# Optimization experiments

Hardware: AMD Instinct MI355X
Metric: run time of the kernel (lower is better)

Reference implementation:

```python
import jax, jax.numpy as jnp
import numpy as np

N = 100_000   # nodes
E = 3_200_000 # directed edges
EC = 16       # edge_channels

def setup_inputs() -> dict:
    key = jax.random.key(0)
    ks = jax.random.split(key, 9)
    x = jax.random.normal(ks[0], (N, 8), jnp.float32)
    adjs = jax.random.randint(ks[1], (2, E), 0, N, jnp.int32)
    edge_attr = jax.random.normal(ks[2], (E, EC), jnp.float32)
    s = 1.0 / np.sqrt(EC)
    lin_e_w = jax.random.uniform(ks[3], (1, EC), jnp.float32, -s, s)
    lin_e_b = jax.random.uniform(ks[4], (1,), jnp.float32, -s, s)
    aggr2_w = jax.random.uniform(ks[5], (1, 4), jnp.float32, -0.5, 0.5)
    aggr2_b = jax.random.uniform(ks[6], (1,), jnp.float32, -0.5, 0.5)
    lin_l_w = jax.random.uniform(ks[7], (1, 1), jnp.float32, -1.0, 1.0)
    lin_l_b = jax.random.uniform(ks[8], (1,), jnp.float32, -1.0, 1.0)
    return dict(x=x, adjs=adjs, edge_attr=edge_attr,
                lin_e_w=lin_e_w, lin_e_b=lin_e_b,
                aggr2_w=aggr2_w, aggr2_b=aggr2_b,
                lin_l_w=lin_l_w, lin_l_b=lin_l_b)

def reference(x, adjs, edge_attr, lin_e_w, lin_e_b, aggr2_w, aggr2_b, lin_l_w, lin_l_b):
    n = x.shape[0]
    # layer 0 (EdgeConv): edge MLP edge_channels -> 1
    ev = (edge_attr @ lin_e_w.T + lin_e_b)[:, 0]            # [E]
    src, dst = adjs[0], adjs[1]
    # to_undirected: edges + reversed edges; row 1 (scatter dest) = cat(dst, src)
    u_idx = jnp.concatenate([dst, src])                      # [2E]
    u_val = jnp.concatenate([ev, ev])                        # [2E]
    cnt = jax.ops.segment_sum(jnp.ones_like(u_val), u_idx, num_segments=n)
    nsum = jax.ops.segment_sum(u_val, u_idx, num_segments=n)
    nmax = jnp.where(cnt > 0, jax.ops.segment_max(u_val, u_idx, num_segments=n), 0.0)
    nmin = jnp.where(cnt > 0, jax.ops.segment_min(u_val, u_idx, num_segments=n), 0.0)
    nmean = nsum / jnp.maximum(cnt, 1.0)                     # torch-scatter mean: 0 for empty

    def inv_clean(node_vals):
        r = 1.0 / node_vals[dst]                             # propagate -> x_i = x[edge_index[1]]
        return jnp.where(jnp.isnan(r) | (r == jnp.inf), 1.0, r)

    nc = jnp.stack([inv_clean(nmax), inv_clean(nmean), inv_clean(nmin), inv_clean(nsum)], axis=1)  # [E,4]
    ec = jnp.where(jnp.isnan(ev) | (ev == jnp.inf), 1.0, ev)[:, None]   # cleaned edge_attr [E,1]
    nc2 = nc @ aggr2_w.T + aggr2_b                            # [E,1]
    out = (ec @ lin_l_w.T + lin_l_b) + nc2 * ec               # [E,1]
    out = jnp.where(out == jnp.inf, 1.0, out)
    return out.reshape(-1)                                    # torch.flatten
```

## Files before the change

kernel.cpp:

```cpp
#include <hip/hip_runtime.h>

#define INF_F (__builtin_inff())
#define PMAX 512
#define G1 1024
#define BT 512
#define BT4 1024
#define NPART 256
#define MARKER 0xFFFFFFFFu
#define LREC 9856


__device__ __forceinline__ unsigned int enc_f(float f) {
    unsigned int u = __float_as_uint(f);
    return (u & 0x80000000u) ? ~u : (u | 0x80000000u);
}
__device__ __forceinline__ float dec_f(unsigned int u) {
    unsigned int b = (u & 0x80000000u) ? (u & 0x7FFFFFFFu) : ~u;
    return __uint_as_float(b);
}
__device__ __forceinline__ float inv_clean(float x) {
    float r = 1.0f / x;
    if (isnan(r) || r == INF_F) r = 1.0f;
    return r;
}
__device__ __forceinline__ float edge_final(float ev, float c, float lw, float lb) {
    float ec = (isnan(ev) || ev == INF_F) ? 1.0f : ev;
    float out = ec * lw + lb + c * ec;
    if (out == INF_F) out = 1.0f;
    return out;
}
__device__ __forceinline__ float dot16_bias(const float* __restrict__ edge_attr,
                                            const float* __restrict__ lin_e_w,
                                            const float* __restrict__ lin_e_b, int e) {
    const float4* ea = reinterpret_cast<const float4*>(edge_attr) + (size_t)e * 4;
    const float4* w4 = reinterpret_cast<const float4*>(lin_e_w);
    float4 a0 = ea[0], a1 = ea[1], a2 = ea[2], a3 = ea[3];
    float4 w0 = w4[0], w1 = w4[1], w2 = w4[2], w3 = w4[3];
    return a0.x * w0.x + a0.y * w0.y + a0.z * w0.z + a0.w * w0.w
         + a1.x * w1.x + a1.y * w1.y + a1.z * w1.z + a1.w * w1.w
         + a2.x * w2.x + a2.y * w2.y + a2.z * w2.z + a2.w * w2.w
         + a3.x * w3.x + a3.y * w3.y + a3.z * w3.z + a3.w * w3.w
         + lin_e_b[0];
}


__global__ void __launch_bounds__(BT)
k1_ev_count(const float* __restrict__ edge_attr,
            const int* __restrict__ src, const int* __restrict__ dst,
            const float* __restrict__ lin_e_w, const float* __restrict__ lin_e_b,
            float* __restrict__ ev_out, unsigned int* __restrict__ gh,
            int E, int P, int CE) {
    __shared__ unsigned int hist[PMAX];
    int t = threadIdx.x, b = blockIdx.x;
    for (int p = t; p < P; p += BT) hist[p] = 0u;
    __syncthreads();
    int start = b * CE, end = min(E, start + CE);
    for (int e = start + t; e < end; e += BT) {
        float ev = dot16_bias(edge_attr, lin_e_w, lin_e_b, e);
        ev_out[e] = ev;
        atomicAdd(&hist[(unsigned int)src[e] >> 8], 1u);
        atomicAdd(&hist[(unsigned int)dst[e] >> 8], 1u);
    }
    __syncthreads();
    for (int p = t; p < P; p += BT) gh[(size_t)b * P + p] = hist[p];
}

__global__ void __launch_bounds__(256)
k2_scan_cols(unsigned int* __restrict__ gh, unsigned int* __restrict__ ptotal, int P) {
    const int VPT = G1 / 256;
    int p = blockIdx.x, t = threadIdx.x;
    unsigned int v[VPT], s = 0u;
    #pragma unroll
    for (int i = 0; i < VPT; ++i) {
        v[i] = (gh[(size_t)(t * VPT + i) * P + p] + 7u) & ~7u;
        s += v[i];
    }
    __shared__ unsigned int sc[256];
    sc[t] = s;
    __syncthreads();
    for (int off = 1; off < 256; off <<= 1) {
        unsigned int x = (t >= off) ? sc[t - off] : 0u;
        __syncthreads();
        sc[t] += x;
        __syncthreads();
    }
    unsigned int run = sc[t] - s;
    #pragma unroll
    for (int i = 0; i < VPT; ++i) {
        gh[(size_t)(t * VPT + i) * P + p] = run;
        run += v[i];
    }
    if (t == 255) ptotal[p] = run;
}

__global__ void k3_scan_part(const unsigned int* __restrict__ ptotal,
                             unsigned int* __restrict__ pbase, int P) {
    int t = threadIdx.x;
    unsigned int u0 = (2 * t < P) ? ptotal[2 * t] : 0u;
    unsigned int u1 = (2 * t + 1 < P) ? ptotal[2 * t + 1] : 0u;
    unsigned int s = u0 + u1;
    __shared__ unsigned int sc[256];
    sc[t] = s;
    __syncthreads();
    for (int off = 1; off < 256; off <<= 1) {
        unsigned int x = (t >= off) ? sc[t - off] : 0u;
        __syncthreads();
        sc[t] += x;
        __syncthreads();
    }
    unsigned int excl = sc[t] - s;
    if (2 * t < P) pbase[2 * t] = excl;
    if (2 * t + 1 < P) pbase[2 * t + 1] = excl + u0;
}

__global__ void __launch_bounds__(BT4)
k4_staged(const int* __restrict__ src, const int* __restrict__ dst,
          const float* __restrict__ ev_in,
          const unsigned int* __restrict__ gh, const unsigned int* __restrict__ pbase,
          const unsigned int* __restrict__ ptotal,
          uint2* __restrict__ rec, int E, int P, int CE) {
    __shared__ uint2 lrec[LREC];
    __shared__ unsigned int lstart[PMAX + 1];
    __shared__ unsigned int lcur[PMAX];
    __shared__ unsigned int goff[PMAX];
    __shared__ unsigned int sc[512];

    const int t = threadIdx.x, b = blockIdx.x;

    for (int p = t; p < P; p += BT4) {
        unsigned int g0 = gh[(size_t)b * P + p];
        unsigned int g1 = (b + 1 < G1) ? gh[(size_t)(b + 1) * P + p] : ptotal[p];
        lcur[p] = g1 - g0;
        goff[p] = pbase[p] + g0;
    }
    __syncthreads();

    unsigned int v = (t < P) ? lcur[t] : 0u;
    if (t < 512) sc[t] = v;
    __syncthreads();
    for (int off = 1; off < 512; off <<= 1) {
        unsigned int x = 0u;
        if (t < 512 && t >= off) x = sc[t - off];
        __syncthreads();
        if (t < 512) sc[t] += x;
        __syncthreads();
    }
    if (t < P) { lstart[t] = sc[t] - v; lcur[t] = sc[t] - v; }
    if (t == P - 1) lstart[P] = sc[t];
    __syncthreads();

    const int start = b * CE, end = min(E, start + CE);
    for (int e = start + t; e < end; e += BT4) {
        float ev = ev_in[e];
        unsigned int ebits = __float_as_uint(ev);
        unsigned int s = (unsigned int)src[e], d = (unsigned int)dst[e];
        unsigned int pos = atomicAdd(&lcur[d >> 8], 1u);
        lrec[pos] = make_uint2(ebits, d & 255u);
        pos = atomicAdd(&lcur[s >> 8], 1u);
        lrec[pos] = make_uint2(ebits, s & 255u);
    }
    __syncthreads();

    for (int p = t; p < P; p += BT4)
        for (unsigned int q = lcur[p]; q < lstart[p + 1]; ++q)
            lrec[q] = make_uint2(0u, MARKER);
    __syncthreads();

    const unsigned int tot = lstart[P];
    for (unsigned int j = t; j < tot; j += BT4) {
        int lo = 0, hi = P;
        while (hi - lo > 1) {
            int mid = (lo + hi) >> 1;
            if (lstart[mid] <= j) lo = mid; else hi = mid;
        }
        rec[goff[lo] + (j - lstart[lo])] = lrec[j];
    }
}

__global__ void __launch_bounds__(1024)
k5_reduce(const uint2* __restrict__ rec,
          const unsigned int* __restrict__ pbase, const unsigned int* __restrict__ ptotal,
          const float* __restrict__ aggr2_w, const float* __restrict__ aggr2_b,
          float* __restrict__ nodeC, int N) {
    __shared__ float ssum[NPART];
    __shared__ unsigned int scnt[NPART], smax[NPART], smin[NPART];
    int p = blockIdx.x, t = threadIdx.x;
    if (t < NPART) { ssum[t] = 0.0f; scnt[t] = 0u; smax[t] = 0u; smin[t] = 0xFFFFFFFFu; }
    __syncthreads();
    unsigned int pb = pbase[p], tot = ptotal[p];
    const uint4* r4 = reinterpret_cast<const uint4*>(rec + pb);
    unsigned int n4 = tot >> 1;
    for (unsigned int i = t; i < n4; i += 1024) {
        uint4 q = r4[i];
        if (q.y != MARKER) {
            float v = __uint_as_float(q.x);
            unsigned int eu = enc_f(v);
            atomicAdd(&ssum[q.y], v);
            atomicAdd(&scnt[q.y], 1u);
            atomicMax(&smax[q.y], eu);
            atomicMin(&smin[q.y], eu);
        }
        if (q.w != MARKER) {
            float v = __uint_as_float(q.z);
            unsigned int eu = enc_f(v);
            atomicAdd(&ssum[q.w], v);
            atomicAdd(&scnt[q.w], 1u);
            atomicMax(&smax[q.w], eu);
            atomicMin(&smin[q.w], eu);
        }
    }
    __syncthreads();
    int node = p * NPART + t;
    if (t < NPART && node < N) {
        unsigned int c = scnt[t];
        float sum = ssum[t];
        float mxv = (c > 0u) ? dec_f(smax[t]) : 0.0f;
        float mnv = (c > 0u) ? dec_f(smin[t]) : 0.0f;
        float mean = sum / fmaxf((float)c, 1.0f);
        float4 w = *reinterpret_cast<const float4*>(aggr2_w);
        nodeC[node] = w.x * inv_clean(mxv) + w.y * inv_clean(mean)
                    + w.z * inv_clean(mnv) + w.w * inv_clean(sum) + aggr2_b[0];
    }
}

__global__ void __launch_bounds__(256)
edge_out(float* __restrict__ evout, const int* __restrict__ dst,
         const float* __restrict__ nodeC,
         const float* __restrict__ lin_l_w, const float* __restrict__ lin_l_b,
         int E) {
    int i = blockIdx.x * blockDim.x + threadIdx.x;
    int base = i * 4;
    float lw = lin_l_w[0], lb = lin_l_b[0];
    if (base + 3 < E) {
        float4 ev = *reinterpret_cast<const float4*>(evout + base);
        int4 d = *reinterpret_cast<const int4*>(dst + base);
        float4 o;
        o.x = edge_final(ev.x, nodeC[d.x], lw, lb);
        o.y = edge_final(ev.y, nodeC[d.y], lw, lb);
        o.z = edge_final(ev.z, nodeC[d.z], lw, lb);
        o.w = edge_final(ev.w, nodeC[d.w], lw, lb);
        *reinterpret_cast<float4*>(evout + base) = o;
    } else {
        for (int e = base; e < E; ++e)
            evout[e] = edge_final(evout[e], nodeC[dst[e]], lw, lb);
    }
}


__global__ void init_nodes_fb(unsigned long long* __restrict__ sc,
                              unsigned int* __restrict__ mx,
                              unsigned int* __restrict__ mn, int total) {
    int i = blockIdx.x * blockDim.x + threadIdx.x;
    if (i < total) { sc[i] = 0ull; mx[i] = 0u; mn[i] = 0xFFFFFFFFu; }
}

__global__ void __launch_bounds__(256)
edge_scatter_fb(const float* __restrict__ edge_attr,
                const int* __restrict__ src, const int* __restrict__ dst,
                const float* __restrict__ lin_e_w, const float* __restrict__ lin_e_b,
                float* __restrict__ ev_out,
                unsigned long long* __restrict__ sc,
                unsigned int* __restrict__ mx, unsigned int* __restrict__ mn,
                int E, int N, int repMask) {
    int e = blockIdx.x * blockDim.x + threadIdx.x;
    if (e >= E) return;
    float ev = dot16_bias(edge_attr, lin_e_w, lin_e_b, e);
    ev_out[e] = ev;
    unsigned long long packed =
        (1ull << 52) | (unsigned long long)((ev + 32.0f) * 1048576.0f);
    unsigned int u = enc_f(ev);
    int base = (blockIdx.x & repMask) * N;
    int s = src[e] + base, d = dst[e] + base;
    atomicAdd(&sc[d], packed);
    atomicAdd(&sc[s], packed);
    atomicMax(&mx[d], u);
    atomicMax(&mx[s], u);
    atomicMin(&mn[d], u);
    atomicMin(&mn[s], u);
}

__global__ void node_combine_fb(const unsigned long long* __restrict__ sc,
                                const unsigned int* __restrict__ mx,
                                const unsigned int* __restrict__ mn,
                                const float* __restrict__ aggr2_w,
                                const float* __restrict__ aggr2_b,
                                float* __restrict__ nodeC, int n, int R) {
    int v = blockIdx.x * blockDim.x + threadIdx.x;
    if (v >= n) return;
    unsigned long long acc = 0ull;
    unsigned int M = 0u, m = 0xFFFFFFFFu;
    for (int r = 0; r < R; ++r) {
        acc += sc[(size_t)r * n + v];
        M = max(M, mx[(size_t)r * n + v]);
        m = min(m, mn[(size_t)r * n + v]);
    }
    unsigned long long icnt = acc >> 52;
    float cnt = (float)icnt;
    double sumfix = (double)(acc & ((1ull << 52) - 1ull));
    float sum = (float)(sumfix * (1.0 / 1048576.0) - 32.0 * (double)icnt);
    float mxv, mnv;
    if (icnt > 0) { mxv = dec_f(M); mnv = dec_f(m); }
    else          { mxv = 0.0f;     mnv = 0.0f; }
    float mean = sum / fmaxf(cnt, 1.0f);
    float4 w = *reinterpret_cast<const float4*>(aggr2_w);
    nodeC[v] = w.x * inv_clean(mxv) + w.y * inv_clean(mean)
             + w.z * inv_clean(mnv) + w.w * inv_clean(sum) + aggr2_b[0];
}

static inline size_t align64(size_t x) { return (x + 63) & ~(size_t)63; }

extern "C" void kernel_launch(void* const* d_in, const int* in_sizes, int n_in,
                              void* d_out, int out_size, void* d_ws, size_t ws_size,
                              hipStream_t stream) {
    const int N = in_sizes[0] / 8;
    const int E = in_sizes[1] / 2;

    const int*   adjs      = (const int*)d_in[1];
    const int*   src       = adjs;
    const int*   dst       = adjs + E;
    const float* edge_attr = (const float*)d_in[2];
    const float* lin_e_w   = (const float*)d_in[3];
    const float* lin_e_b   = (const float*)d_in[4];
    const float* aggr2_w   = (const float*)d_in[5];
    const float* aggr2_b   = (const float*)d_in[6];
    const float* lin_l_w   = (const float*)d_in[7];
    const float* lin_l_b   = (const float*)d_in[8];
    float* out = (float*)d_out;

    char* ws = (char*)d_ws;

    const int P = (N + NPART - 1) / NPART;
    const int CE = (E + G1 - 1) / G1;

    size_t max_rec = (size_t)2 * E + (size_t)G1 * P * 8;
    size_t off_gh = 0;
    size_t off_pt = align64(off_gh + (size_t)G1 * P * 4);
    size_t off_pb = align64(off_pt + (size_t)PMAX * 4);
    size_t off_rc = align64(off_pb + (size_t)PMAX * 4);
    size_t off_nc = align64(off_rc + max_rec * 8);
    size_t need_sort = off_nc + (size_t)N * 4;

    bool lds_ok = ((size_t)2 * CE + (size_t)7 * P) <= LREC;

    if (P <= PMAX && lds_ok && ws_size >= need_sort) {
        unsigned int* gh     = (unsigned int*)(ws + off_gh);
        unsigned int* ptotal = (unsigned int*)(ws + off_pt);
        unsigned int* pbase  = (unsigned int*)(ws + off_pb);
        uint2*        rec    = (uint2*)(ws + off_rc);
        float*        nodeC  = (float*)(ws + off_nc);

        hipLaunchKernelGGL(k1_ev_count, dim3(G1), dim3(BT), 0, stream,
                           edge_attr, src, dst, lin_e_w, lin_e_b, out, gh, E, P, CE);
        hipLaunchKernelGGL(k2_scan_cols, dim3(P), dim3(256), 0, stream, gh, ptotal, P);
        hipLaunchKernelGGL(k3_scan_part, dim3(1), dim3(256), 0, stream, ptotal, pbase, P);
        hipLaunchKernelGGL(k4_staged, dim3(G1), dim3(BT4), 0, stream,
                           src, dst, out, gh, pbase, ptotal, rec, E, P, CE);
        hipLaunchKernelGGL(k5_reduce, dim3(P), dim3(1024), 0, stream,
                           rec, pbase, ptotal, aggr2_w, aggr2_b, nodeC, N);
        int nt = (E + 3) / 4;
        hipLaunchKernelGGL(edge_out, dim3((nt + 255) / 256), dim3(256), 0, stream,
                           out, dst, nodeC, lin_l_w, lin_l_b, E);
    } else {
        int R = 8;
        while (R > 1 && (size_t)R * N * 16 + (size_t)N * 4 > ws_size) R >>= 1;
        unsigned long long* sc    = (unsigned long long*)ws;
        unsigned int*       mx    = (unsigned int*)(sc + (size_t)R * N);
        unsigned int*       mn    = mx + (size_t)R * N;
        float*              nodeC = (float*)(mn + (size_t)R * N);

        int totalRN = R * N;
        hipLaunchKernelGGL(init_nodes_fb, dim3((totalRN + 255) / 256), dim3(256), 0, stream,
                           sc, mx, mn, totalRN);
        hipLaunchKernelGGL(edge_scatter_fb, dim3((E + 255) / 256), dim3(256), 0, stream,
                           edge_attr, src, dst, lin_e_w, lin_e_b,
                           out, sc, mx, mn, E, N, R - 1);
        hipLaunchKernelGGL(node_combine_fb, dim3((N + 255) / 256), dim3(256), 0, stream,
                           sc, mx, mn, aggr2_w, aggr2_b, nodeC, N, R);
        int nt = (E + 3) / 4;
        hipLaunchKernelGGL(edge_out, dim3((nt + 255) / 256), dim3(256), 0, stream,
                           out, dst, nodeC, lin_l_w, lin_l_b, E);
    }
}
```

Before: 167.1 us.

## Restructure partitioned sort with global atomic bucket reservation and fused ev/stage kernel

Replaces the per-block histogram matrix, column scan and second pass with a lightweight global histogram kernel, a single small scan, and a fused kernel. The fused kernel computes edge values, counts locally, reserves padded slots per partition with a global atomic cursor, and writes records from LDS with one wavefront per partition. This removes the G1×P histogram traffic and the re-read of ev/src/dst between kernels, and drops the per-record binary search. In exchange, record order within a partition is no longer deterministic, more padding is reserved per partition, and the old path is kept only as a fallback.

```diff
diff --git a/kernel.cpp b/kernel.cpp
--- a/kernel.cpp
+++ b/kernel.cpp
@@ -2,11 +2,18 @@
 
 #define INF_F (__builtin_inff())
 #define PMAX 512
+#define NPART 256
+#define MARKER 0xFFFFFFFFu
+#define CSTRIDE 16
+
+#define GB 1024
+#define TB 1024
+#define THH 512
+#define LRECB 6252
+
 #define G1 1024
 #define BT 512
 #define BT4 1024
-#define NPART 256
-#define MARKER 0xFFFFFFFFu
 #define LREC 9856
 
 
@@ -44,98 +51,84 @@
 }
 
 
-__global__ void __launch_bounds__(BT)
-k1_ev_count(const float* __restrict__ edge_attr,
+__global__ void kz_zero(unsigned int* __restrict__ gtotal, int P) {
+    int t = threadIdx.x;
+    if (t < P) gtotal[t * CSTRIDE] = 0u;
+}
+
+__global__ void __launch_bounds__(THH)
+kh_hist(const int* __restrict__ src, const int* __restrict__ dst,
+        unsigned int* __restrict__ gtotal, int E, int P, int CE) {
+    __shared__ unsigned int hist[PMAX];
+    int t = threadIdx.x, b = blockIdx.x;
+    for (int p = t; p < P; p += THH) hist[p] = 0u;
+    __syncthreads();
+    int start = b * CE, end = min(E, start + CE);
+    for (int e = start + t; e < end; e += THH) {
+        atomicAdd(&hist[(unsigned int)src[e] >> 8], 1u);
+        atomicAdd(&hist[(unsigned int)dst[e] >> 8], 1u);
+    }
+    __syncthreads();
+    for (int p = t; p < P; p += THH)
+        if (hist[p]) atomicAdd(&gtotal[p * CSTRIDE], hist[p]);
+}
+
+__global__ void __launch_bounds__(512)
+ks_scan(const unsigned int* __restrict__ gtotal, unsigned int* __restrict__ pbase,
+        unsigned int* __restrict__ gcur, int P) {
+    __shared__ unsigned int sc[512];
+    int t = threadIdx.x;
+    unsigned int v = 0u;
+    if (t < P) v = ((gtotal[t * CSTRIDE] + 7u) & ~7u) + 7u * GB;
+    sc[t] = v;
+    __syncthreads();
+    for (int off = 1; off < 512; off <<= 1) {
+        unsigned int x = (t >= off) ? sc[t - off] : 0u;
+        __syncthreads();
+        sc[t] += x;
+        __syncthreads();
+    }
+    if (t < P) {
+        unsigned int excl = sc[t] - v;
+        pbase[t] = excl;
+        gcur[t * CSTRIDE] = excl;
+    }
+}
+
+__global__ void __launch_bounds__(TB)
+kb_ev_stage(const float* __restrict__ edge_attr,
             const int* __restrict__ src, const int* __restrict__ dst,
             const float* __restrict__ lin_e_w, const float* __restrict__ lin_e_b,
-            float* __restrict__ ev_out, unsigned int* __restrict__ gh,
-            int E, int P, int CE) {
-    __shared__ unsigned int hist[PMAX];
-    int t = threadIdx.x, b = blockIdx.x;
-    for (int p = t; p < P; p += BT) hist[p] = 0u;
-    __syncthreads();
-    int start = b * CE, end = min(E, start + CE);
-    for (int e = start + t; e < end; e += BT) {
-        float ev = dot16_bias(edge_attr, lin_e_w, lin_e_b, e);
-        ev_out[e] = ev;
-        atomicAdd(&hist[(unsigned int)src[e] >> 8], 1u);
-        atomicAdd(&hist[(unsigned int)dst[e] >> 8], 1u);
-    }
-    __syncthreads();
-    for (int p = t; p < P; p += BT) gh[(size_t)b * P + p] = hist[p];
-}
-
-__global__ void __launch_bounds__(256)
-k2_scan_cols(unsigned int* __restrict__ gh, unsigned int* __restrict__ ptotal, int P) {
-    const int VPT = G1 / 256;
-    int p = blockIdx.x, t = threadIdx.x;
-    unsigned int v[VPT], s = 0u;
+            float* __restrict__ ev_out, unsigned int* __restrict__ gcur,
+            uint2* __restrict__ rec, int E, int P, int CE) {
+    __shared__ uint2 lrec[LRECB];
+    __shared__ unsigned int sc[512];
+    __shared__ unsigned int lcnt[PMAX], lstart[PMAX], lcur[PMAX], lgb[PMAX];
+
+    const int t = threadIdx.x, b = blockIdx.x;
+    const int start = b * CE, end = min(E, start + CE);
+
+    for (int p = t; p < P; p += TB) lcnt[p] = 0u;
+    __syncthreads();
+
+    int es[4], ed[4];
+    float ee[4];
     #pragma unroll
-    for (int i = 0; i < VPT; ++i) {
-        v[i] = (gh[(size_t)(t * VPT + i) * P + p] + 7u) & ~7u;
-        s += v[i];
-    }
-    __shared__ unsigned int sc[256];
-    sc[t] = s;
-    __syncthreads();
-    for (int off = 1; off < 256; off <<= 1) {
-        unsigned int x = (t >= off) ? sc[t - off] : 0u;
-        __syncthreads();
-        sc[t] += x;
-        __syncthreads();
-    }
-    unsigned int run = sc[t] - s;
-    #pragma unroll
-    for (int i = 0; i < VPT; ++i) {
-        gh[(size_t)(t * VPT + i) * P + p] = run;
-        run += v[i];
-    }
-    if (t == 255) ptotal[p] = run;
-}
-
-__global__ void k3_scan_part(const unsigned int* __restrict__ ptotal,
-                             unsigned int* __restrict__ pbase, int P) {
-    int t = threadIdx.x;
-    unsigned int u0 = (2 * t < P) ? ptotal[2 * t] : 0u;
-    unsigned int u1 = (2 * t + 1 < P) ? ptotal[2 * t + 1] : 0u;
-    unsigned int s = u0 + u1;
-    __shared__ unsigned int sc[256];
-    sc[t] = s;
-    __syncthreads();
-    for (int off = 1; off < 256; off <<= 1) {
-        unsigned int x = (t >= off) ? sc[t - off] : 0u;
-        __syncthreads();
-        sc[t] += x;
-        __syncthreads();
-    }
-    unsigned int excl = sc[t] - s;
-    if (2 * t < P) pbase[2 * t] = excl;
-    if (2 * t + 1 < P) pbase[2 * t + 1] = excl + u0;
-}
-
-__global__ void __launch_bounds__(BT4)
-k4_staged(const int* __restrict__ src, const int* __restrict__ dst,
-          const float* __restrict__ ev_in,
-          const unsigned int* __restrict__ gh, const unsigned int* __restrict__ pbase,
-          const unsigned int* __restrict__ ptotal,
-          uint2* __restrict__ rec, int E, int P, int CE) {
-    __shared__ uint2 lrec[LREC];
-    __shared__ unsigned int lstart[PMAX + 1];
-    __shared__ unsigned int lcur[PMAX];
-    __shared__ unsigned int goff[PMAX];
-    __shared__ unsigned int sc[512];
-
-    const int t = threadIdx.x, b = blockIdx.x;
-
-    for (int p = t; p < P; p += BT4) {
-        unsigned int g0 = gh[(size_t)b * P + p];
-        unsigned int g1 = (b + 1 < G1) ? gh[(size_t)(b + 1) * P + p] : ptotal[p];
-        lcur[p] = g1 - g0;
-        goff[p] = pbase[p] + g0;
-    }
-    __syncthreads();
-
-    unsigned int v = (t < P) ? lcur[t] : 0u;
+    for (int i = 0; i < 4; ++i) {
+        int e = start + i * TB + t;
+        int s = 0, d = 0; float ev = 0.0f;
+        if (e < end) {
+            s = src[e]; d = dst[e];
+            ev = dot16_bias(edge_attr, lin_e_w, lin_e_b, e);
+            ev_out[e] = ev;
+            atomicAdd(&lcnt[(unsigned int)s >> 8], 1u);
+            atomicAdd(&lcnt[(unsigned int)d >> 8], 1u);
+        }
+        es[i] = s; ed[i] = d; ee[i] = ev;
+    }
+    __syncthreads();
+
+    unsigned int v = (t < 512) ? ((t < P) ? lcnt[t] : 0u) : 0u;
     if (t < 512) sc[t] = v;
     __syncthreads();
     for (int off = 1; off < 512; off <<= 1) {
@@ -146,40 +139,39 @@
         __syncthreads();
     }
     if (t < P) { lstart[t] = sc[t] - v; lcur[t] = sc[t] - v; }
-    if (t == P - 1) lstart[P] = sc[t];
-    __syncthreads();
-
-    const int start = b * CE, end = min(E, start + CE);
-    for (int e = start + t; e < end; e += BT4) {
-        float ev = ev_in[e];
-        unsigned int ebits = __float_as_uint(ev);
-        unsigned int s = (unsigned int)src[e], d = (unsigned int)dst[e];
-        unsigned int pos = atomicAdd(&lcur[d >> 8], 1u);
-        lrec[pos] = make_uint2(ebits, d & 255u);
-        pos = atomicAdd(&lcur[s >> 8], 1u);
-        lrec[pos] = make_uint2(ebits, s & 255u);
-    }
-    __syncthreads();
-
-    for (int p = t; p < P; p += BT4)
-        for (unsigned int q = lcur[p]; q < lstart[p + 1]; ++q)
-            lrec[q] = make_uint2(0u, MARKER);
-    __syncthreads();
-
-    const unsigned int tot = lstart[P];
-    for (unsigned int j = t; j < tot; j += BT4) {
-        int lo = 0, hi = P;
-        while (hi - lo > 1) {
-            int mid = (lo + hi) >> 1;
-            if (lstart[mid] <= j) lo = mid; else hi = mid;
-        }
-        rec[goff[lo] + (j - lstart[lo])] = lrec[j];
+    __syncthreads();
+
+    if (t < P && lcnt[t])
+        lgb[t] = atomicAdd(&gcur[t * CSTRIDE], (lcnt[t] + 7u) & ~7u);
+
+    #pragma unroll
+    for (int i = 0; i < 4; ++i) {
+        int e = start + i * TB + t;
+        if (e < end) {
+            unsigned int ebits = __float_as_uint(ee[i]);
+            unsigned int s = (unsigned int)es[i], d = (unsigned int)ed[i];
+            unsigned int pos = atomicAdd(&lcur[d >> 8], 1u);
+            lrec[pos] = make_uint2(ebits, d & 255u);
+            pos = atomicAdd(&lcur[s >> 8], 1u);
+            lrec[pos] = make_uint2(ebits, s & 255u);
+        }
+    }
+    __syncthreads();
+
+    const int wv = t >> 6, lane = t & 63;
+    for (int p = wv; p < P; p += TB / 64) {
+        unsigned int rcnt = lcnt[p];
+        if (!rcnt) continue;
+        unsigned int base = lgb[p], ls = lstart[p];
+        unsigned int padded = (rcnt + 7u) & ~7u;
+        for (unsigned int j = lane; j < padded; j += 64)
+            rec[base + j] = (j < rcnt) ? lrec[ls + j] : make_uint2(0u, MARKER);
     }
 }
 
 __global__ void __launch_bounds__(1024)
-k5_reduce(const uint2* __restrict__ rec,
-          const unsigned int* __restrict__ pbase, const unsigned int* __restrict__ ptotal,
+kr_reduce(const uint2* __restrict__ rec,
+          const unsigned int* __restrict__ pbase, const unsigned int* __restrict__ gcur,
           const float* __restrict__ aggr2_w, const float* __restrict__ aggr2_b,
           float* __restrict__ nodeC, int N) {
     __shared__ float ssum[NPART];
@@ -187,9 +179,10 @@
     int p = blockIdx.x, t = threadIdx.x;
     if (t < NPART) { ssum[t] = 0.0f; scnt[t] = 0u; smax[t] = 0u; smin[t] = 0xFFFFFFFFu; }
     __syncthreads();
-    unsigned int pb = pbase[p], tot = ptotal[p];
+    unsigned int pb = pbase[p];
+    unsigned int pe = gcur[p * CSTRIDE];
     const uint4* r4 = reinterpret_cast<const uint4*>(rec + pb);
-    unsigned int n4 = tot >> 1;
+    unsigned int n4 = (pe - pb) >> 1;
     for (unsigned int i = t; i < n4; i += 1024) {
         uint4 q = r4[i];
         if (q.y != MARKER) {
@@ -247,64 +240,178 @@
 }
 
 
-__global__ void init_nodes_fb(unsigned long long* __restrict__ sc,
-                              unsigned int* __restrict__ mx,
-                              unsigned int* __restrict__ mn, int total) {
-    int i = blockIdx.x * blockDim.x + threadIdx.x;
-    if (i < total) { sc[i] = 0ull; mx[i] = 0u; mn[i] = 0xFFFFFFFFu; }
+__global__ void __launch_bounds__(BT)
+k1_ev_count(const float* __restrict__ edge_attr,
+            const int* __restrict__ src, const int* __restrict__ dst,
+            const float* __restrict__ lin_e_w, const float* __restrict__ lin_e_b,
+            float* __restrict__ ev_out, unsigned int* __restrict__ gh,
+            int E, int P, int CE) {
+    __shared__ unsigned int hist[PMAX];
+    int t = threadIdx.x, b = blockIdx.x;
+    for (int p = t; p < P; p += BT) hist[p] = 0u;
+    __syncthreads();
+    int start = b * CE, end = min(E, start + CE);
+    for (int e = start + t; e < end; e += BT) {
+        float ev = dot16_bias(edge_attr, lin_e_w, lin_e_b, e);
+        ev_out[e] = ev;
+        atomicAdd(&hist[(unsigned int)src[e] >> 8], 1u);
+        atomicAdd(&hist[(unsigned int)dst[e] >> 8], 1u);
+    }
+    __syncthreads();
+    for (int p = t; p < P; p += BT) gh[(size_t)b * P + p] = hist[p];
 }
 
 __global__ void __launch_bounds__(256)
-edge_scatter_fb(const float* __restrict__ edge_attr,
-                const int* __restrict__ src, const int* __restrict__ dst,
-                const float* __restrict__ lin_e_w, const float* __restrict__ lin_e_b,
-                float* __restrict__ ev_out,
-                unsigned long long* __restrict__ sc,
-                unsigned int* __restrict__ mx, unsigned int* __restrict__ mn,
-                int E, int N, int repMask) {
-    int e = blockIdx.x * blockDim.x + threadIdx.x;
-    if (e >= E) return;
-    float ev = dot16_bias(edge_attr, lin_e_w, lin_e_b, e);
-    ev_out[e] = ev;
-    unsigned long long packed =
-        (1ull << 52) | (unsigned long long)((ev + 32.0f) * 1048576.0f);
-    unsigned int u = enc_f(ev);
-    int base = (blockIdx.x & repMask) * N;
-    int s = src[e] + base, d = dst[e] + base;
-    atomicAdd(&sc[d], packed);
-    atomicAdd(&sc[s], packed);
-    atomicMax(&mx[d], u);
-    atomicMax(&mx[s], u);
-    atomicMin(&mn[d], u);
-    atomicMin(&mn[s], u);
-}
-
-__global__ void node_combine_fb(const unsigned long long* __restrict__ sc,
-                                const unsigned int* __restrict__ mx,
-                                const unsigned int* __restrict__ mn,
-                                const float* __restrict__ aggr2_w,
-                                const float* __restrict__ aggr2_b,
-                                float* __restrict__ nodeC, int n, int R) {
-    int v = blockIdx.x * blockDim.x + threadIdx.x;
-    if (v >= n) return;
-    unsigned long long acc = 0ull;
-    unsigned int M = 0u, m = 0xFFFFFFFFu;
-    for (int r = 0; r < R; ++r) {
-        acc += sc[(size_t)r * n + v];
-        M = max(M, mx[(size_t)r * n + v]);
-        m = min(m, mn[(size_t)r * n + v]);
-    }
-    unsigned long long icnt = acc >> 52;
-    float cnt = (float)icnt;
-    double sumfix = (double)(acc & ((1ull << 52) - 1ull));
-    float sum = (float)(sumfix * (1.0 / 1048576.0) - 32.0 * (double)icnt);
-    float mxv, mnv;
-    if (icnt > 0) { mxv = dec_f(M); mnv = dec_f(m); }
-    else          { mxv = 0.0f;     mnv = 0.0f; }
-    float mean = sum / fmaxf(cnt, 1.0f);
-    float4 w = *reinterpret_cast<const float4*>(aggr2_w);
-    nodeC[v] = w.x * inv_clean(mxv) + w.y * inv_clean(mean)
-             + w.z * inv_clean(mnv) + w.w * inv_clean(sum) + aggr2_b[0];
+k2_scan_cols(unsigned int* __restrict__ gh, unsigned int* __restrict__ ptotal, int P) {
+    const int VPT = G1 / 256;
+    int p = blockIdx.x, t = threadIdx.x;
+    unsigned int v[VPT], s = 0u;
+    #pragma unroll
+    for (int i = 0; i < VPT; ++i) {
+        v[i] = (gh[(size_t)(t * VPT + i) * P + p] + 7u) & ~7u;
+        s += v[i];
+    }
+    __shared__ unsigned int sc[256];
+    sc[t] = s;
+    __syncthreads();
+    for (int off = 1; off < 256; off <<= 1) {
+        unsigned int x = (t >= off) ? sc[t - off] : 0u;
+        __syncthreads();
+        sc[t] += x;
+        __syncthreads();
+    }
+    unsigned int run = sc[t] - s;
+    #pragma unroll
+    for (int i = 0; i < VPT; ++i) {
+        gh[(size_t)(t * VPT + i) * P + p] = run;
+        run += v[i];
+    }
+    if (t == 255) ptotal[p] = run;
+}
+
+__global__ void k3_scan_part(const unsigned int* __restrict__ ptotal,
+                             unsigned int* __restrict__ pbase, int P) {
+    int t = threadIdx.x;
+    unsigned int u0 = (2 * t < P) ? ptotal[2 * t] : 0u;
+    unsigned int u1 = (2 * t + 1 < P) ? ptotal[2 * t + 1] : 0u;
+    unsigned int s = u0 + u1;
+    __shared__ unsigned int sc[256];
+    sc[t] = s;
+    __syncthreads();
+    for (int off = 1; off < 256; off <<= 1) {
+        unsigned int x = (t >= off) ? sc[t - off] : 0u;
+        __syncthreads();
+        sc[t] += x;
+        __syncthreads();
+    }
+    unsigned int excl = sc[t] - s;
+    if (2 * t < P) pbase[2 * t] = excl;
+    if (2 * t + 1 < P) pbase[2 * t + 1] = excl + u0;
+}
+
+__global__ void __launch_bounds__(BT4)
+k4_staged(const int* __restrict__ src, const int* __restrict__ dst,
+          const float* __restrict__ ev_in,
+          const unsigned int* __restrict__ gh, const unsigned int* __restrict__ pbase,
+          const unsigned int* __restrict__ ptotal,
+          uint2* __restrict__ rec, int E, int P, int CE) {
+    __shared__ uint2 lrec[LREC];
+    __shared__ unsigned int lstart[PMAX + 1];
+    __shared__ unsigned int lcur[PMAX];
+    __shared__ unsigned int goff[PMAX];
+    __shared__ unsigned int sc[512];
+
+    const int t = threadIdx.x, b = blockIdx.x;
+    for (int p = t; p < P; p += BT4) {
+        unsigned int g0 = gh[(size_t)b * P + p];
+        unsigned int g1 = (b + 1 < G1) ? gh[(size_t)(b + 1) * P + p] : ptotal[p];
+        lcur[p] = g1 - g0;
+        goff[p] = pbase[p] + g0;
+    }
+    __syncthreads();
+    unsigned int v = (t < P) ? lcur[t] : 0u;
+    if (t < 512) sc[t] = v;
+    __syncthreads();
+    for (int off = 1; off < 512; off <<= 1) {
+        unsigned int x = 0u;
+        if (t < 512 && t >= off) x = sc[t - off];
+        __syncthreads();
+        if (t < 512) sc[t] += x;
+        __syncthreads();
+    }
+    if (t < P) { lstart[t] = sc[t] - v; lcur[t] = sc[t] - v; }
+    if (t == P - 1) lstart[P] = sc[t];
+    __syncthreads();
+    const int start = b * CE, end = min(E, start + CE);
+    for (int e = start + t; e < end; e += BT4) {
+        float ev = ev_in[e];
+        unsigned int ebits = __float_as_uint(ev);
+        unsigned int s = (unsigned int)src[e], d = (unsigned int)dst[e];
+        unsigned int pos = atomicAdd(&lcur[d >> 8], 1u);
+        lrec[pos] = make_uint2(ebits, d & 255u);
+        pos = atomicAdd(&lcur[s >> 8], 1u);
+        lrec[pos] = make_uint2(ebits, s & 255u);
+    }
+    __syncthreads();
+    for (int p = t; p < P; p += BT4)
+        for (unsigned int q = lcur[p]; q < lstart[p + 1]; ++q)
+            lrec[q] = make_uint2(0u, MARKER);
+    __syncthreads();
+    const unsigned int tot = lstart[P];
+    for (unsigned int j = t; j < tot; j += BT4) {
+        int lo = 0, hi = P;
+        while (hi - lo > 1) {
+            int mid = (lo + hi) >> 1;
+            if (lstart[mid] <= j) lo = mid; else hi = mid;
+        }
+        rec[goff[lo] + (j - lstart[lo])] = lrec[j];
+    }
+}
+
+__global__ void __launch_bounds__(1024)
+k5_reduce(const uint2* __restrict__ rec,
+          const unsigned int* __restrict__ pbase, const unsigned int* __restrict__ ptotal,
+          const float* __restrict__ aggr2_w, const float* __restrict__ aggr2_b,
+          float* __restrict__ nodeC, int N) {
+    __shared__ float ssum[NPART];
+    __shared__ unsigned int scnt[NPART], smax[NPART], smin[NPART];
+    int p = blockIdx.x, t = threadIdx.x;
+    if (t < NPART) { ssum[t] = 0.0f; scnt[t] = 0u; smax[t] = 0u; smin[t] = 0xFFFFFFFFu; }
+    __syncthreads();
+    unsigned int pb = pbase[p], tot = ptotal[p];
+    const uint4* r4 = reinterpret_cast<const uint4*>(rec + pb);
+    unsigned int n4 = tot >> 1;
+    for (unsigned int i = t; i < n4; i += 1024) {
+        uint4 q = r4[i];
+        if (q.y != MARKER) {
+            float v = __uint_as_float(q.x);
+            unsigned int eu = enc_f(v);
+            atomicAdd(&ssum[q.y], v);
+            atomicAdd(&scnt[q.y], 1u);
+            atomicMax(&smax[q.y], eu);
+            atomicMin(&smin[q.y], eu);
+        }
+        if (q.w != MARKER) {
+            float v = __uint_as_float(q.z);
+            unsigned int eu = enc_f(v);
+            atomicAdd(&ssum[q.w], v);
+            atomicAdd(&scnt[q.w], 1u);
+            atomicMax(&smax[q.w], eu);
+            atomicMin(&smin[q.w], eu);
+        }
+    }
+    __syncthreads();
+    int node = p * NPART + t;
+    if (t < NPART && node < N) {
+        unsigned int c = scnt[t];
+        float sum = ssum[t];
+        float mxv = (c > 0u) ? dec_f(smax[t]) : 0.0f;
+        float mnv = (c > 0u) ? dec_f(smin[t]) : 0.0f;
+        float mean = sum / fmaxf((float)c, 1.0f);
+        float4 w = *reinterpret_cast<const float4*>(aggr2_w);
+        nodeC[node] = w.x * inv_clean(mxv) + w.y * inv_clean(mean)
+                    + w.z * inv_clean(mnv) + w.w * inv_clean(sum) + aggr2_b[0];
+    }
 }
 
 static inline size_t align64(size_t x) { return (x + 63) & ~(size_t)63; }
@@ -328,56 +435,64 @@
     float* out = (float*)d_out;
 
     char* ws = (char*)d_ws;
-
     const int P = (N + NPART - 1) / NPART;
+
+    const int CEb = (E + GB - 1) / GB;
+    size_t rec_cap = (size_t)2 * E + (size_t)P * (7u * GB + 8u) + 64;
+    size_t n_gt = 0;
+    size_t n_pb = align64(n_gt + (size_t)PMAX * CSTRIDE * 4);
+    size_t n_gc = align64(n_pb + (size_t)PMAX * 4);
+    size_t n_rc = align64(n_gc + (size_t)PMAX * CSTRIDE * 4);
+    size_t n_nc = align64(n_rc + rec_cap * 8);
+    size_t need_new = n_nc + (size_t)N * 4;
+
+    if (P <= PMAX && 2 * CEb <= LRECB && ws_size >= need_new) {
+        unsigned int* gtotal = (unsigned int*)(ws + n_gt);
+        unsigned int* pbase  = (unsigned int*)(ws + n_pb);
+        unsigned int* gcur   = (unsigned int*)(ws + n_gc);
+        uint2*        rec    = (uint2*)(ws + n_rc);
+        float*        nodeC  = (float*)(ws + n_nc);
+
+        const int CEh = (E + GB - 1) / GB;
+        hipLaunchKernelGGL(kz_zero, dim3(1), dim3(512), 0, stream, gtotal, P);
+        hipLaunchKernelGGL(kh_hist, dim3(GB), dim3(THH), 0, stream,
+                           src, dst, gtotal, E, P, CEh);
+        hipLaunchKernelGGL(ks_scan, dim3(1), dim3(512), 0, stream,
+                           gtotal, pbase, gcur, P);
+        hipLaunchKernelGGL(kb_ev_stage, dim3(GB), dim3(TB), 0, stream,
+                           edge_attr, src, dst, lin_e_w, lin_e_b,
+                           out, gcur, rec, E, P, CEb);
+        hipLaunchKernelGGL(kr_reduce, dim3(P), dim3(1024), 0, stream,
+                           rec, pbase, gcur, aggr2_w, aggr2_b, nodeC, N);
+        int nt = (E + 3) / 4;
+        hipLaunchKernelGGL(edge_out, dim3((nt + 255) / 256), dim3(256), 0, stream,
+                           out, dst, nodeC, lin_l_w, lin_l_b, E);
+        return;
+    }
+
     const int CE = (E + G1 - 1) / G1;
-
     size_t max_rec = (size_t)2 * E + (size_t)G1 * P * 8;
     size_t off_gh = 0;
     size_t off_pt = align64(off_gh + (size_t)G1 * P * 4);
     size_t off_pb = align64(off_pt + (size_t)PMAX * 4);
     size_t off_rc = align64(off_pb + (size_t)PMAX * 4);
     size_t off_nc = align64(off_rc + max_rec * 8);
-    size_t need_sort = off_nc + (size_t)N * 4;
-
-    bool lds_ok = ((size_t)2 * CE + (size_t)7 * P) <= LREC;
-
-    if (P <= PMAX && lds_ok && ws_size >= need_sort) {
-        unsigned int* gh     = (unsigned int*)(ws + off_gh);
-        unsigned int* ptotal = (unsigned int*)(ws + off_pt);
-        unsigned int* pbase  = (unsigned int*)(ws + off_pb);
-        uint2*        rec    = (uint2*)(ws + off_rc);
-        float*        nodeC  = (float*)(ws + off_nc);
-
-        hipLaunchKernelGGL(k1_ev_count, dim3(G1), dim3(BT), 0, stream,
-                           edge_attr, src, dst, lin_e_w, lin_e_b, out, gh, E, P, CE);
-        hipLaunchKernelGGL(k2_scan_cols, dim3(P), dim3(256), 0, stream, gh, ptotal, P);
-        hipLaunchKernelGGL(k3_scan_part, dim3(1), dim3(256), 0, stream, ptotal, pbase, P);
-        hipLaunchKernelGGL(k4_staged, dim3(G1), dim3(BT4), 0, stream,
-                           src, dst, out, gh, pbase, ptotal, rec, E, P, CE);
-        hipLaunchKernelGGL(k5_reduce, dim3(P), dim3(1024), 0, stream,
-                           rec, pbase, ptotal, aggr2_w, aggr2_b, nodeC, N);
-        int nt = (E + 3) / 4;
-        hipLaunchKernelGGL(edge_out, dim3((nt + 255) / 256), dim3(256), 0, stream,
-                           out, dst, nodeC, lin_l_w, lin_l_b, E);
-    } else {
-        int R = 8;
-        while (R > 1 && (size_t)R * N * 16 + (size_t)N * 4 > ws_size) R >>= 1;
-        unsigned long long* sc    = (unsigned long long*)ws;
-        unsigned int*       mx    = (unsigned int*)(sc + (size_t)R * N);
-        unsigned int*       mn    = mx + (size_t)R * N;
-        float*              nodeC = (float*)(mn + (size_t)R * N);
-
-        int totalRN = R * N;
-        hipLaunchKernelGGL(init_nodes_fb, dim3((totalRN + 255) / 256), dim3(256), 0, stream,
-                           sc, mx, mn, totalRN);
-        hipLaunchKernelGGL(edge_scatter_fb, dim3((E + 255) / 256), dim3(256), 0, stream,
-                           edge_attr, src, dst, lin_e_w, lin_e_b,
-                           out, sc, mx, mn, E, N, R - 1);
-        hipLaunchKernelGGL(node_combine_fb, dim3((N + 255) / 256), dim3(256), 0, stream,
-                           sc, mx, mn, aggr2_w, aggr2_b, nodeC, N, R);
-        int nt = (E + 3) / 4;
-        hipLaunchKernelGGL(edge_out, dim3((nt + 255) / 256), dim3(256), 0, stream,
-                           out, dst, nodeC, lin_l_w, lin_l_b, E);
-    }
-}
+
+    unsigned int* gh     = (unsigned int*)(ws + off_gh);
+    unsigned int* ptotal = (unsigned int*)(ws + off_pt);
+    unsigned int* pbase  = (unsigned int*)(ws + off_pb);
+    uint2*        rec    = (uint2*)(ws + off_rc);
+    float*        nodeC  = (float*)(ws + off_nc);
+
+    hipLaunchKernelGGL(k1_ev_count, dim3(G1), dim3(BT), 0, stream,
+                       edge_attr, src, dst, lin_e_w, lin_e_b, out, gh, E, P, CE);
+    hipLaunchKernelGGL(k2_scan_cols, dim3(P), dim3(256), 0, stream, gh, ptotal, P);
+    hipLaunchKernelGGL(k3_scan_part, dim3(1), dim3(256), 0, stream, ptotal, pbase, P);
+    hipLaunchKernelGGL(k4_staged, dim3(G1), dim3(BT4), 0, stream,
+                       src, dst, out, gh, pbase, ptotal, rec, E, P, CE);
+    hipLaunchKernelGGL(k5_reduce, dim3(P), dim3(1024), 0, stream,
+                       rec, pbase, ptotal, aggr2_w, aggr2_b, nodeC, N);
+    int nt = (E + 3) / 4;
+    hipLaunchKernelGGL(edge_out, dim3((nt + 255) / 256), dim3(256), 0, stream,
+                       out, dst, nodeC, lin_l_w, lin_l_b, E);
+}
```

New measurement: 172.0 us. +2.9%, slower.
